# Kernel optimization log

Hardware: AMD Instinct MI355X
Metric: run time of the kernel (lower is better)

## Reference

```python
import jax, jax.numpy as jnp
import numpy as np

N, E, F, H, G = 50000, 640000, 128, 128, 64


def setup_inputs() -> dict:
    key = jax.random.key(0)
    ks = jax.random.split(key, 10)
    x = jax.random.normal(ks[0], (N, F), dtype=jnp.float32)
    edge_index = jax.random.randint(ks[1], (2, E), 0, N)
    batch = jnp.sort(jax.random.randint(ks[2], (N,), 0, G))

    def glorot(k, shp):
        return jax.random.normal(k, shp, dtype=jnp.float32) * np.float32(1.0 / np.sqrt(shp[0]))

    W1 = glorot(ks[3], (F, H)); b1 = jnp.zeros((H,), jnp.float32)
    W2 = glorot(ks[4], (H, H)); b2 = jnp.zeros((H,), jnp.float32)
    W3 = glorot(ks[5], (H, H)); b3 = jnp.zeros((H,), jnp.float32)
    W4 = glorot(ks[6], (H, 2)); b4 = jnp.zeros((2,), jnp.float32)
    return {"x": x, "W1": W1, "b1": b1, "W2": W2, "b2": b2,
            "W3": W3, "b3": b3, "W4": W4, "b4": b4,
            "edge_index": edge_index, "batch": batch, "num_graphs": G}


def reference(x, W1, b1, W2, b2, W3, b3, W4, b4, edge_index, batch, num_graphs):
    n = x.shape[0]
    loop = jnp.arange(n, dtype=edge_index.dtype)
    src = jnp.concatenate([edge_index[0], loop])  # with self-loops (PyG GCNConv default)
    dst = jnp.concatenate([edge_index[1], loop])
    # symmetric degree normalization: D^{-1/2} (A+I) D^{-1/2}
    deg = jax.ops.segment_sum(jnp.ones_like(src, dtype=x.dtype), dst, num_segments=n)
    dinv = jnp.where(deg > 0, jax.lax.rsqrt(deg), 0.0)
    norm = (dinv[src] * dinv[dst])[:, None]  # [E+N, 1]

    def gcn_conv(h, W, b):
        m = h @ W                                   # transform first (F->H), then propagate
        agg = jax.ops.segment_sum(m[src] * norm, dst, num_segments=n)
        return agg + b

    h = jax.nn.relu(gcn_conv(x, W1, b1))
    h = jax.nn.relu(gcn_conv(h, W2, b2))
    g = jax.ops.segment_max(h, batch, num_segments=num_graphs)  # global_max_pool
    z = jax.nn.relu(g @ W3 + b3)                    # dropout is identity in eval
    logits = z @ W4 + b4
    return jax.nn.log_softmax(logits, axis=1)
```

## Files before the change

kernel.cpp:

```cpp
#include <hip/hip_runtime.h>
#include <hip/hip_bf16.h>
#include <math.h>

#define HDIM 128
#define SCAN_B 256
#define NBLK 256

typedef short bfrag __attribute__((ext_vector_type(8)));
typedef float f32x4 __attribute__((ext_vector_type(4)));

__device__ inline unsigned short f2bf_rne(float x) {
    unsigned u = __float_as_uint(x);
    u = (u + 0x7fffu + ((u >> 16) & 1u)) >> 16;
    return (unsigned short)u;
}
__device__ inline float bf_lo(unsigned u) { return __uint_as_float(u << 16); }
__device__ inline float bf_hi(unsigned u) { return __uint_as_float(u & 0xffff0000u); }
__device__ inline unsigned bf_pack(float lo, float hi) {
    return ((unsigned)f2bf_rne(hi) << 16) | (unsigned)f2bf_rne(lo);
}


__device__ inline void hist_body(int b, const int* __restrict__ dst,
                                 int* __restrict__ hist, int E, int chunk, int nbuck) {
    __shared__ int hl[256];
    int t = threadIdx.x;
    hl[t] = 0;
    __syncthreads();
    int start = b * chunk, end = min(E, start + chunk);
    for (int e = start + t; e < end; e += 256) atomicAdd(&hl[dst[e] >> 8], 1);
    __syncthreads();
    if (t < nbuck) hist[t * NBLK + b] = hl[t];
}

__device__ inline void wfrag_body(int b, const float* __restrict__ W1,
                                  const float* __restrict__ W2,
                                  unsigned short* __restrict__ w1h,
                                  unsigned short* __restrict__ w1l,
                                  unsigned short* __restrict__ w2h,
                                  unsigned short* __restrict__ w2l) {
    const float* W = (b < 64) ? W1 : W2;
    unsigned short* whi = (b < 64) ? w1h : w2h;
    unsigned short* wlo = (b < 64) ? w1l : w2l;
    int idx = (b & 63) * 256 + threadIdx.x;
    int k = idx >> 7;
    int n = idx & 127;
    int kt = k >> 5, q = (k >> 3) & 3, j = k & 7;
    int lm = n >> 3, nt = n & 7;
    int lane = q * 16 + lm;
    int o = ((kt * 8 + nt) * 64 + lane) * 8 + j;
    float x = W[idx];
    unsigned short hb = f2bf_rne(x);
    float hf = __uint_as_float(((unsigned)hb) << 16);
    unsigned short lb = f2bf_rne(x - hf);
    whi[o] = hb;
    wlo[o] = lb;
}

__device__ inline void scatter_body(int b, const int* __restrict__ srcv,
                                    const int* __restrict__ dstv,
                                    const int* __restrict__ hscan,
                                    int2* __restrict__ sorted,
                                    int E, int chunk, int nbuck) {
    __shared__ int cur[256];
    int t = threadIdx.x;
    if (t < nbuck) cur[t] = hscan[t * NBLK + b];
    __syncthreads();
    int start = b * chunk, end = min(E, start + chunk);
    for (int e = start + t; e < end; e += 256) {
        int d = dstv[e];
        int pos = atomicAdd(&cur[d >> 8], 1);
        sorted[pos] = make_int2(srcv[e], d);
    }
}

#define GBM 64
__device__ inline void gemm_f32_body(int b, const float* __restrict__ A,
                                     const unsigned short* __restrict__ whi,
                                     const unsigned short* __restrict__ wlo,
                                     unsigned short* __restrict__ C, int Nrows) {
    int tid = threadIdx.x;
    int w = tid >> 6, L = tid & 63;
    int lm = L & 15, lq = L >> 4;
    int row0 = b * GBM + w * 16;

    f32x4 acc[8];
#pragma unroll
    for (int nt = 0; nt < 8; ++nt) acc[nt] = (f32x4)(0.f);

#pragma unroll
    for (int kt = 0; kt < 4; ++kt) {
        int gr = row0 + lm;
        float4 v0 = make_float4(0.f, 0.f, 0.f, 0.f);
        float4 v1 = v0;
        if (gr < Nrows) {
            const float* p = &A[(size_t)gr * HDIM + kt * 32 + lq * 8];
            v0 = *(const float4*)p;
            v1 = *(const float4*)(p + 4);
        }
        float xv[8] = {v0.x, v0.y, v0.z, v0.w, v1.x, v1.y, v1.z, v1.w};
        bfrag ah, al;
#pragma unroll
        for (int j = 0; j < 8; ++j) {
            float x = xv[j];
            unsigned short hb = f2bf_rne(x);
            float hf = __uint_as_float(((unsigned)hb) << 16);
            unsigned short lb = f2bf_rne(x - hf);
            ah[j] = (short)hb;
            al[j] = (short)lb;
        }
#pragma unroll
        for (int nt = 0; nt < 8; ++nt) {
            int o = ((kt * 8 + nt) * 64 + L) * 8;
            bfrag wh = *(const bfrag*)&whi[o];
            bfrag wl = *(const bfrag*)&wlo[o];
            acc[nt] = __builtin_amdgcn_mfma_f32_16x16x32_bf16(ah, wh, acc[nt], 0, 0, 0);
            acc[nt] = __builtin_amdgcn_mfma_f32_16x16x32_bf16(al, wh, acc[nt], 0, 0, 0);
            acc[nt] = __builtin_amdgcn_mfma_f32_16x16x32_bf16(ah, wl, acc[nt], 0, 0, 0);
        }
    }

#pragma unroll
    for (int i = 0; i < 4; ++i) {
        int gr = row0 + lq * 4 + i;
        if (gr < Nrows) {
            bfrag e;
#pragma unroll
            for (int nt = 0; nt < 8; ++nt) e[nt] = (short)f2bf_rne(acc[nt][i]);
            *(bfrag*)&C[(size_t)gr * HDIM + lm * 8] = e;
        }
    }
}

__global__ __launch_bounds__(256) void mega1_kernel(const int* __restrict__ dst,
                                                    int* __restrict__ hist, int E,
                                                    int chunk, int nbuck,
                                                    const float* __restrict__ W1,
                                                    const float* __restrict__ W2,
                                                    unsigned short* __restrict__ w1h,
                                                    unsigned short* __restrict__ w1l,
                                                    unsigned short* __restrict__ w2h,
                                                    unsigned short* __restrict__ w2l) {
    int b = blockIdx.x;
    if (b < NBLK) hist_body(b, dst, hist, E, chunk, nbuck);
    else wfrag_body(b - NBLK, W1, W2, w1h, w1l, w2h, w2l);
}

__global__ __launch_bounds__(256) void mega3_kernel(const int* __restrict__ srcv,
                                                    const int* __restrict__ dstv,
                                                    const int* __restrict__ hscan,
                                                    int2* __restrict__ sorted,
                                                    int E, int chunk, int nbuck,
                                                    const float* __restrict__ A,
                                                    const unsigned short* __restrict__ whi,
                                                    const unsigned short* __restrict__ wlo,
                                                    unsigned short* __restrict__ C, int Nrows) {
    int b = blockIdx.x;
    if (b < NBLK) scatter_body(b, srcv, dstv, hscan, sorted, E, chunk, nbuck);
    else gemm_f32_body(b - NBLK, A, whi, wlo, C, Nrows);
}

__global__ __launch_bounds__(SCAN_B) void scan1_kernel(const int* __restrict__ in,
                                                       int* __restrict__ out,
                                                       int* __restrict__ sums, int n) {
    __shared__ int s[SCAN_B];
    int t = threadIdx.x;
    int idx = blockIdx.x * SCAN_B + t;
    int v = (idx < n) ? in[idx] : 0;
    s[t] = v;
    __syncthreads();
    for (int off = 1; off < SCAN_B; off <<= 1) {
        int x = (t >= off) ? s[t - off] : 0;
        __syncthreads();
        s[t] += x;
        __syncthreads();
    }
    if (idx < n) out[idx] = s[t];
    if (t == SCAN_B - 1) sums[blockIdx.x] = s[t];
}

__global__ __launch_bounds__(SCAN_B) void scan2_kernel(int* __restrict__ sums, int nb) {
    __shared__ int s[SCAN_B];
    int t = threadIdx.x;
    int v = (t < nb) ? sums[t] : 0;
    s[t] = v;
    __syncthreads();
    for (int off = 1; off < SCAN_B; off <<= 1) {
        int x = (t >= off) ? s[t - off] : 0;
        __syncthreads();
        s[t] += x;
        __syncthreads();
    }
    if (t < nb) sums[t] = s[t] - v;
}

__global__ __launch_bounds__(SCAN_B) void scan3_kernel(const int* __restrict__ in,
                                                       int* __restrict__ out,
                                                       const int* __restrict__ sums, int n) {
    int idx = blockIdx.x * SCAN_B + threadIdx.x;
    if (idx < n) out[idx] = out[idx] - in[idx] + sums[blockIdx.x];
}

__global__ __launch_bounds__(256) void csr_kernel(const int2* __restrict__ sorted,
                                                  const int* __restrict__ hscan,
                                                  int* __restrict__ rowstart,
                                                  float* __restrict__ dinv,
                                                  int* __restrict__ csr,
                                                  int N, int E, int nbuck) {
    __shared__ int cnt[256];
    __shared__ int s[256];
    __shared__ int cur[256];
    int b = blockIdx.x;
    int t = threadIdx.x;
    int start = hscan[b * NBLK];
    int end = (b + 1 < nbuck) ? hscan[(b + 1) * NBLK] : E;
    cnt[t] = 0;
    __syncthreads();
    for (int e = start + t; e < end; e += 256)
        atomicAdd(&cnt[sorted[e].y & 255], 1);
    __syncthreads();
    int v = cnt[t];
    s[t] = v;
    __syncthreads();
    for (int off = 1; off < 256; off <<= 1) {
        int x = (t >= off) ? s[t - off] : 0;
        __syncthreads();
        s[t] += x;
        __syncthreads();
    }
    int excl = s[t] - v;
    int node = b * 256 + t;
    if (node < N) {
        rowstart[node] = start + excl;
        dinv[node] = rsqrtf((float)(v + 1));
    }
    if (b == nbuck - 1 && t == 0) rowstart[N] = E;
    cur[t] = start + excl;
    __syncthreads();
    for (int e = start + t; e < end; e += 256) {
        int2 ed = sorted[e];
        int pos = atomicAdd(&cur[ed.y & 255], 1);
        csr[pos] = ed.x;
    }
}

#define QACC(UV, WT)                                   \
    acc[0] = fmaf(WT, bf_lo((UV).x), acc[0]);          \
    acc[1] = fmaf(WT, bf_hi((UV).x), acc[1]);          \
    acc[2] = fmaf(WT, bf_lo((UV).y), acc[2]);          \
    acc[3] = fmaf(WT, bf_hi((UV).y), acc[3]);          \
    acc[4] = fmaf(WT, bf_lo((UV).z), acc[4]);          \
    acc[5] = fmaf(WT, bf_hi((UV).z), acc[5]);          \
    acc[6] = fmaf(WT, bf_lo((UV).w), acc[6]);          \
    acc[7] = fmaf(WT, bf_hi((UV).w), acc[7]);

__device__ inline void qgather(const uint4* __restrict__ m4,
                               const int* __restrict__ csr,
                               const float* __restrict__ dinv,
                               int p, int pend, int t, float* acc) {
    for (; p + 8 <= pend; p += 8) {
        int s0 = csr[p], s1 = csr[p + 1], s2 = csr[p + 2], s3 = csr[p + 3];
        int s4 = csr[p + 4], s5 = csr[p + 5], s6 = csr[p + 6], s7 = csr[p + 7];
        float w0 = dinv[s0], w1 = dinv[s1], w2 = dinv[s2], w3 = dinv[s3];
        float w4 = dinv[s4], w5 = dinv[s5], w6 = dinv[s6], w7 = dinv[s7];
        uint4 u0 = m4[(size_t)s0 * 16 + t];
        uint4 u1 = m4[(size_t)s1 * 16 + t];
        uint4 u2 = m4[(size_t)s2 * 16 + t];
        uint4 u3 = m4[(size_t)s3 * 16 + t];
        uint4 u4 = m4[(size_t)s4 * 16 + t];
        uint4 u5 = m4[(size_t)s5 * 16 + t];
        uint4 u6 = m4[(size_t)s6 * 16 + t];
        uint4 u7 = m4[(size_t)s7 * 16 + t];
        QACC(u0, w0); QACC(u1, w1); QACC(u2, w2); QACC(u3, w3);
        QACC(u4, w4); QACC(u5, w5); QACC(u6, w6); QACC(u7, w7);
    }
    if (p + 4 <= pend) {
        int s0 = csr[p], s1 = csr[p + 1], s2 = csr[p + 2], s3 = csr[p + 3];
        float w0 = dinv[s0], w1 = dinv[s1], w2 = dinv[s2], w3 = dinv[s3];
        uint4 u0 = m4[(size_t)s0 * 16 + t];
        uint4 u1 = m4[(size_t)s1 * 16 + t];
        uint4 u2 = m4[(size_t)s2 * 16 + t];
        uint4 u3 = m4[(size_t)s3 * 16 + t];
        QACC(u0, w0); QACC(u1, w1); QACC(u2, w2); QACC(u3, w3);
        p += 4;
    }
    if (p + 2 <= pend) {
        int s0 = csr[p], s1 = csr[p + 1];
        float w0 = dinv[s0], w1 = dinv[s1];
        uint4 u0 = m4[(size_t)s0 * 16 + t];
        uint4 u1 = m4[(size_t)s1 * 16 + t];
        QACC(u0, w0); QACC(u1, w1);
        p += 2;
    }
    if (p < pend) {
        int s0 = csr[p];
        float w0 = dinv[s0];
        uint4 u0 = m4[(size_t)s0 * 16 + t];
        QACC(u0, w0);
    }
}

__global__ __launch_bounds__(256) void agg_gemm_kernel(
        const uint4* __restrict__ m4,
        const int* __restrict__ rowstart,
        const int* __restrict__ csr,
        const float* __restrict__ dinv,
        const float* __restrict__ bias,
        const unsigned short* __restrict__ whi,
        const unsigned short* __restrict__ wlo,
        uint4* __restrict__ out_m, int n) {
    __shared__ unsigned short hbuf[16][HDIM + 8];
    __shared__ float cbuf[16][HDIM + 4];
    int t = threadIdx.x & 15;
    int nl = threadIdx.x >> 4;
    int node = blockIdx.x * 16 + nl;

    unsigned short hv[8] = {0, 0, 0, 0, 0, 0, 0, 0};
    if (node < n) {
        float dd = dinv[node];
        float acc[8];
        uint4 u = m4[(size_t)node * 16 + t];
        acc[0] = dd * bf_lo(u.x); acc[1] = dd * bf_hi(u.x);
        acc[2] = dd * bf_lo(u.y); acc[3] = dd * bf_hi(u.y);
        acc[4] = dd * bf_lo(u.z); acc[5] = dd * bf_hi(u.z);
        acc[6] = dd * bf_lo(u.w); acc[7] = dd * bf_hi(u.w);
        qgather(m4, csr, dinv, rowstart[node], rowstart[node + 1], t, acc);
        float4 b0 = *(const float4*)&bias[t * 8];
        float4 b1 = *(const float4*)&bias[t * 8 + 4];
        float bb[8] = {b0.x, b0.y, b0.z, b0.w, b1.x, b1.y, b1.z, b1.w};
#pragma unroll
        for (int j = 0; j < 8; ++j)
            hv[j] = f2bf_rne(fmaxf(fmaf(dd, acc[j], bb[j]), 0.f));
    }
    *(uint4*)&hbuf[nl][t * 8] = *(uint4*)hv;
    __syncthreads();

    int w = threadIdx.x >> 6, L = threadIdx.x & 63;
    int lm = L & 15, lq = L >> 4;
    f32x4 acc2[2];
    acc2[0] = (f32x4)(0.f);
    acc2[1] = (f32x4)(0.f);
#pragma unroll
    for (int kt = 0; kt < 4; ++kt) {
        bfrag a = *(const bfrag*)&hbuf[lm][kt * 32 + lq * 8];
#pragma unroll
        for (int q2 = 0; q2 < 2; ++q2) {
            int nt = w * 2 + q2;
            int o = ((kt * 8 + nt) * 64 + L) * 8;
            bfrag wh = *(const bfrag*)&whi[o];
            bfrag wl = *(const bfrag*)&wlo[o];
            acc2[q2] = __builtin_amdgcn_mfma_f32_16x16x32_bf16(a, wh, acc2[q2], 0, 0, 0);
            acc2[q2] = __builtin_amdgcn_mfma_f32_16x16x32_bf16(a, wl, acc2[q2], 0, 0, 0);
        }
    }
#pragma unroll
    for (int q2 = 0; q2 < 2; ++q2) {
        int nt = w * 2 + q2;
#pragma unroll
        for (int i = 0; i < 4; ++i) cbuf[lq * 4 + i][lm * 8 + nt] = acc2[q2][i];
    }
    __syncthreads();

    if (node < n) {
        float4 r0 = *(const float4*)&cbuf[nl][t * 8];
        float4 r1 = *(const float4*)&cbuf[nl][t * 8 + 4];
        unsigned short ev[8];
        ev[0] = f2bf_rne(r0.x); ev[1] = f2bf_rne(r0.y);
        ev[2] = f2bf_rne(r0.z); ev[3] = f2bf_rne(r0.w);
        ev[4] = f2bf_rne(r1.x); ev[5] = f2bf_rne(r1.y);
        ev[6] = f2bf_rne(r1.z); ev[7] = f2bf_rne(r1.w);
        out_m[(size_t)node * 16 + t] = *(uint4*)ev;
    }
}

__global__ __launch_bounds__(256) void agg_pool_kernel(const uint4* __restrict__ m4,
                                                       const int* __restrict__ rowstart,
                                                       const int* __restrict__ csr,
                                                       const float* __restrict__ dinv,
                                                       const float* __restrict__ bias,
                                                       const int* __restrict__ batch,
                                                       unsigned int* __restrict__ g, int n) {
    __shared__ float smx[16][HDIM];
    __shared__ int sgid[16];
    int t = threadIdx.x & 15;
    int nl = threadIdx.x >> 4;
    int node = blockIdx.x * 16 + nl;
    bool valid = node < n;
    if (valid) {
        float dd = dinv[node];
        float acc[8];
        uint4 u = m4[(size_t)node * 16 + t];
        acc[0] = dd * bf_lo(u.x); acc[1] = dd * bf_hi(u.x);
        acc[2] = dd * bf_lo(u.y); acc[3] = dd * bf_hi(u.y);
        acc[4] = dd * bf_lo(u.z); acc[5] = dd * bf_hi(u.z);
        acc[6] = dd * bf_lo(u.w); acc[7] = dd * bf_hi(u.w);
        qgather(m4, csr, dinv, rowstart[node], rowstart[node + 1], t, acc);
        float4 b0 = *(const float4*)&bias[t * 8];
        float4 b1 = *(const float4*)&bias[t * 8 + 4];
        float4 r0, r1;
        r0.x = fmaxf(fmaf(dd, acc[0], b0.x), 0.f);
        r0.y = fmaxf(fmaf(dd, acc[1], b0.y), 0.f);
        r0.z = fmaxf(fmaf(dd, acc[2], b0.z), 0.f);
        r0.w = fmaxf(fmaf(dd, acc[3], b0.w), 0.f);
        r1.x = fmaxf(fmaf(dd, acc[4], b1.x), 0.f);
        r1.y = fmaxf(fmaf(dd, acc[5], b1.y), 0.f);
        r1.z = fmaxf(fmaf(dd, acc[6], b1.z), 0.f);
        r1.w = fmaxf(fmaf(dd, acc[7], b1.w), 0.f);
        *(float4*)&smx[nl][t * 8] = r0;
        *(float4*)&smx[nl][t * 8 + 4] = r1;
    }
    if (t == 0) sgid[nl] = valid ? batch[node] : -1;
    __syncthreads();
    if (threadIdx.x < HDIM) {
        int c = threadIdx.x;
        int curg = -1;
        float run = 0.f;
#pragma unroll
        for (int r = 0; r < 16; ++r) {
            int gg = sgid[r];
            if (gg < 0) continue;
            if (gg != curg) {
                if (curg >= 0) atomicMax(&g[curg * HDIM + c], __float_as_uint(run));
                curg = gg;
                run = smx[r][c];
            } else {
                run = fmaxf(run, smx[r][c]);
            }
        }
        if (curg >= 0) atomicMax(&g[curg * HDIM + c], __float_as_uint(run));
    }
}

__global__ __launch_bounds__(128) void mlp_kernel(const unsigned int* __restrict__ gbits,
                                                  const float* __restrict__ W3,
                                                  const float* __restrict__ b3,
                                                  const float* __restrict__ W4,
                                                  const float* __restrict__ b4,
                                                  float* __restrict__ out) {
    __shared__ float gs[HDIM];
    __shared__ float r0[HDIM];
    __shared__ float r1[HDIM];
    int j = threadIdx.x;
    int b = blockIdx.x;
    gs[j] = __uint_as_float(gbits[b * HDIM + j]);
    __syncthreads();
    float acc = b3[j];
#pragma unroll 8
    for (int k = 0; k < HDIM; ++k) acc = fmaf(gs[k], W3[k * HDIM + j], acc);
    float z = fmaxf(acc, 0.f);
    r0[j] = z * W4[j * 2 + 0];
    r1[j] = z * W4[j * 2 + 1];
    __syncthreads();
    for (int off = 64; off > 0; off >>= 1) {
        if (j < off) {
            r0[j] += r0[j + off];
            r1[j] += r1[j + off];
        }
        __syncthreads();
    }
    if (j == 0) {
        float l0 = r0[0] + b4[0];
        float l1 = r1[0] + b4[1];
        float mx = fmaxf(l0, l1);
        float lse = mx + logf(expf(l0 - mx) + expf(l1 - mx));
        out[b * 2 + 0] = l0 - lse;
        out[b * 2 + 1] = l1 - lse;
    }
}

extern "C" void kernel_launch(void* const* d_in, const int* in_sizes, int n_in,
                              void* d_out, int out_size, void* d_ws, size_t ws_size,
                              hipStream_t stream) {
    const float* x  = (const float*)d_in[0];
    const float* W1 = (const float*)d_in[1];
    const float* b1 = (const float*)d_in[2];
    const float* W2 = (const float*)d_in[3];
    const float* b2 = (const float*)d_in[4];
    const float* W3 = (const float*)d_in[5];
    const float* b3 = (const float*)d_in[6];
    const float* W4 = (const float*)d_in[7];
    const float* b4 = (const float*)d_in[8];
    const int* ei    = (const int*)d_in[9];
    const int* batch = (const int*)d_in[10];

    const int N = in_sizes[0] / HDIM;
    const int E = in_sizes[9] / 2;
    const int G = out_size / 2;
    const int* src = ei;
    const int* dst = ei + E;

    const int nbuck = (N + 255) >> 8;
    const int nscan = nbuck * NBLK;
    const int chunk = (E + NBLK - 1) / NBLK;

    const int Nr = ((N + 63) / 64) * 64;
    char* wsb = (char*)d_ws;
    size_t o = 0;
    unsigned int* g = (unsigned int*)(wsb + o); o += (size_t)G * HDIM * 4;
    size_t zero_bytes = o;
    int* hist = (int*)(wsb + o);           o += (size_t)nscan * 4;
    int* hscan = (int*)(wsb + o);          o += (size_t)nscan * 4;
    int* sums = (int*)(wsb + o);           o += 256 * 4;
    int* rowstart = (int*)(wsb + o);       o += (size_t)(Nr + 64) * 4;
    float* dinv = (float*)(wsb + o);       o += (size_t)Nr * 4;
    int2* sorted = (int2*)(wsb + o);       o += (size_t)E * 8;
    int* csr = (int*)(wsb + o);            o += (size_t)E * 4;
    unsigned short* wf1h = (unsigned short*)(wsb + o); o += (size_t)HDIM * HDIM * 2;
    unsigned short* wf1l = (unsigned short*)(wsb + o); o += (size_t)HDIM * HDIM * 2;
    unsigned short* wf2h = (unsigned short*)(wsb + o); o += (size_t)HDIM * HDIM * 2;
    unsigned short* wf2l = (unsigned short*)(wsb + o); o += (size_t)HDIM * HDIM * 2;
    unsigned short* m = (unsigned short*)(wsb + o);    o += (size_t)Nr * HDIM * 2;
    unsigned short* m2 = (unsigned short*)(wsb + o);   o += (size_t)Nr * HDIM * 2;
    (void)ws_size; (void)n_in;

    (void)hipMemsetAsync(d_ws, 0, zero_bytes, stream);

    int sblocks = (nscan + SCAN_B - 1) / SCAN_B;
    int gemm_blocks = (N + GBM - 1) / GBM;
    int agg_blocks = (N + 15) / 16;

    mega1_kernel<<<NBLK + 128, 256, 0, stream>>>(dst, hist, E, chunk, nbuck,
                                                 W1, W2, wf1h, wf1l, wf2h, wf2l);
    scan1_kernel<<<sblocks, SCAN_B, 0, stream>>>(hist, hscan, sums, nscan);
    scan2_kernel<<<1, SCAN_B, 0, stream>>>(sums, sblocks);
    scan3_kernel<<<sblocks, SCAN_B, 0, stream>>>(hist, hscan, sums, nscan);
    mega3_kernel<<<NBLK + gemm_blocks, 256, 0, stream>>>(src, dst, hscan, sorted,
                                                         E, chunk, nbuck,
                                                         x, wf1h, wf1l, m, N);
    csr_kernel<<<nbuck, 256, 0, stream>>>(sorted, hscan, rowstart, dinv, csr, N, E, nbuck);
    agg_gemm_kernel<<<agg_blocks, 256, 0, stream>>>((const uint4*)m, rowstart, csr,
                                                    dinv, b1, wf2h, wf2l,
                                                    (uint4*)m2, N);
    agg_pool_kernel<<<agg_blocks, 256, 0, stream>>>((const uint4*)m2, rowstart, csr,
                                                    dinv, b2, batch, g, N);
    mlp_kernel<<<G, 128, 0, stream>>>(g, W3, b3, W4, b4, (float*)d_out);
}
```

Baseline: 201.4 us.

## Build CSR with direct global atomics and prescale messages by source dinv

```diff
diff --git a/kernel.cpp b/kernel.cpp
--- a/kernel.cpp
+++ b/kernel.cpp
@@ -16,21 +16,13 @@
 }
 __device__ inline float bf_lo(unsigned u) { return __uint_as_float(u << 16); }
 __device__ inline float bf_hi(unsigned u) { return __uint_as_float(u & 0xffff0000u); }
-__device__ inline unsigned bf_pack(float lo, float hi) {
-    return ((unsigned)f2bf_rne(hi) << 16) | (unsigned)f2bf_rne(lo);
-}
 
 
 __device__ inline void hist_body(int b, const int* __restrict__ dst,
-                                 int* __restrict__ hist, int E, int chunk, int nbuck) {
-    __shared__ int hl[256];
-    int t = threadIdx.x;
-    hl[t] = 0;
-    __syncthreads();
+                                 int* __restrict__ hist, int E, int chunk) {
     int start = b * chunk, end = min(E, start + chunk);
-    for (int e = start + t; e < end; e += 256) atomicAdd(&hl[dst[e] >> 8], 1);
-    __syncthreads();
-    if (t < nbuck) hist[t * NBLK + b] = hl[t];
+    for (int e = start + threadIdx.x; e < end; e += 256)
+        atomicAdd(&hist[dst[e]], 1);
 }
 
 __device__ inline void wfrag_body(int b, const float* __restrict__ W1,
@@ -59,18 +51,13 @@
 
 __device__ inline void scatter_body(int b, const int* __restrict__ srcv,
                                     const int* __restrict__ dstv,
-                                    const int* __restrict__ hscan,
-                                    int2* __restrict__ sorted,
-                                    int E, int chunk, int nbuck) {
-    __shared__ int cur[256];
-    int t = threadIdx.x;
-    if (t < nbuck) cur[t] = hscan[t * NBLK + b];
-    __syncthreads();
+                                    int* __restrict__ cursor,
+                                    int* __restrict__ csr,
+                                    int E, int chunk) {
     int start = b * chunk, end = min(E, start + chunk);
-    for (int e = start + t; e < end; e += 256) {
-        int d = dstv[e];
-        int pos = atomicAdd(&cur[d >> 8], 1);
-        sorted[pos] = make_int2(srcv[e], d);
+    for (int e = start + threadIdx.x; e < end; e += 256) {
+        int pos = atomicAdd(&cursor[dstv[e]], 1);
+        csr[pos] = srcv[e];
     }
 }
 
@@ -78,6 +65,7 @@
 __device__ inline void gemm_f32_body(int b, const float* __restrict__ A,
                                      const unsigned short* __restrict__ whi,
                                      const unsigned short* __restrict__ wlo,
+                                     const float* __restrict__ dinv,
                                      unsigned short* __restrict__ C, int Nrows) {
     int tid = threadIdx.x;
     int w = tid >> 6, L = tid & 63;
@@ -124,9 +112,10 @@
     for (int i = 0; i < 4; ++i) {
         int gr = row0 + lq * 4 + i;
         if (gr < Nrows) {
+            float dd = dinv[gr];
             bfrag e;
 #pragma unroll
-            for (int nt = 0; nt < 8; ++nt) e[nt] = (short)f2bf_rne(acc[nt][i]);
+            for (int nt = 0; nt < 8; ++nt) e[nt] = (short)f2bf_rne(dd * acc[nt][i]);
             *(bfrag*)&C[(size_t)gr * HDIM + lm * 8] = e;
         }
     }
@@ -134,7 +123,7 @@
 
 __global__ __launch_bounds__(256) void mega1_kernel(const int* __restrict__ dst,
                                                     int* __restrict__ hist, int E,
-                                                    int chunk, int nbuck,
+                                                    int chunk,
                                                     const float* __restrict__ W1,
                                                     const float* __restrict__ W2,
                                                     unsigned short* __restrict__ w1h,
@@ -142,22 +131,23 @@
                                                     unsigned short* __restrict__ w2h,
                                                     unsigned short* __restrict__ w2l) {
     int b = blockIdx.x;
-    if (b < NBLK) hist_body(b, dst, hist, E, chunk, nbuck);
+    if (b < NBLK) hist_body(b, dst, hist, E, chunk);
     else wfrag_body(b - NBLK, W1, W2, w1h, w1l, w2h, w2l);
 }
 
 __global__ __launch_bounds__(256) void mega3_kernel(const int* __restrict__ srcv,
                                                     const int* __restrict__ dstv,
-                                                    const int* __restrict__ hscan,
-                                                    int2* __restrict__ sorted,
-                                                    int E, int chunk, int nbuck,
+                                                    int* __restrict__ cursor,
+                                                    int* __restrict__ csr,
+                                                    int E, int chunk,
                                                     const float* __restrict__ A,
                                                     const unsigned short* __restrict__ whi,
                                                     const unsigned short* __restrict__ wlo,
+                                                    const float* __restrict__ dinv,
                                                     unsigned short* __restrict__ C, int Nrows) {
     int b = blockIdx.x;
-    if (b < NBLK) scatter_body(b, srcv, dstv, hscan, sorted, E, chunk, nbuck);
-    else gemm_f32_body(b - NBLK, A, whi, wlo, C, Nrows);
+    if (b < NBLK) scatter_body(b, srcv, dstv, cursor, csr, E, chunk);
+    else gemm_f32_body(b - NBLK, A, whi, wlo, dinv, C, Nrows);
 }
 
 __global__ __launch_bounds__(SCAN_B) void scan1_kernel(const int* __restrict__ in,
@@ -179,90 +169,46 @@
     if (t == SCAN_B - 1) sums[blockIdx.x] = s[t];
 }
 
-__global__ __launch_bounds__(SCAN_B) void scan2_kernel(int* __restrict__ sums, int nb) {
+__global__ __launch_bounds__(SCAN_B) void scan3_kernel(const int* __restrict__ in,
+                                                       const int* __restrict__ incl,
+                                                       const int* __restrict__ sums,
+                                                       int* __restrict__ rowstart,
+                                                       int* __restrict__ cursor,
+                                                       float* __restrict__ dinv,
+                                                       int n, int E) {
     __shared__ int s[SCAN_B];
     int t = threadIdx.x;
-    int v = (t < nb) ? sums[t] : 0;
-    s[t] = v;
-    __syncthreads();
-    for (int off = 1; off < SCAN_B; off <<= 1) {
-        int x = (t >= off) ? s[t - off] : 0;
+    int b = blockIdx.x;
+    s[t] = (t < b) ? sums[t] : 0;
+    __syncthreads();
+    for (int off = SCAN_B / 2; off > 0; off >>= 1) {
+        if (t < off) s[t] += s[t + off];
         __syncthreads();
-        s[t] += x;
-        __syncthreads();
-    }
-    if (t < nb) sums[t] = s[t] - v;
-}
-
-__global__ __launch_bounds__(SCAN_B) void scan3_kernel(const int* __restrict__ in,
-                                                       int* __restrict__ out,
-                                                       const int* __restrict__ sums, int n) {
-    int idx = blockIdx.x * SCAN_B + threadIdx.x;
-    if (idx < n) out[idx] = out[idx] - in[idx] + sums[blockIdx.x];
-}
-
-__global__ __launch_bounds__(256) void csr_kernel(const int2* __restrict__ sorted,
-                                                  const int* __restrict__ hscan,
-                                                  int* __restrict__ rowstart,
-                                                  float* __restrict__ dinv,
-                                                  int* __restrict__ csr,
-                                                  int N, int E, int nbuck) {
-    __shared__ int cnt[256];
-    __shared__ int s[256];
-    __shared__ int cur[256];
-    int b = blockIdx.x;
-    int t = threadIdx.x;
-    int start = hscan[b * NBLK];
-    int end = (b + 1 < nbuck) ? hscan[(b + 1) * NBLK] : E;
-    cnt[t] = 0;
-    __syncthreads();
-    for (int e = start + t; e < end; e += 256)
-        atomicAdd(&cnt[sorted[e].y & 255], 1);
-    __syncthreads();
-    int v = cnt[t];
-    s[t] = v;
-    __syncthreads();
-    for (int off = 1; off < 256; off <<= 1) {
-        int x = (t >= off) ? s[t - off] : 0;
-        __syncthreads();
-        s[t] += x;
-        __syncthreads();
-    }
-    int excl = s[t] - v;
-    int node = b * 256 + t;
-    if (node < N) {
-        rowstart[node] = start + excl;
-        dinv[node] = rsqrtf((float)(v + 1));
-    }
-    if (b == nbuck - 1 && t == 0) rowstart[N] = E;
-    cur[t] = start + excl;
-    __syncthreads();
-    for (int e = start + t; e < end; e += 256) {
-        int2 ed = sorted[e];
-        int pos = atomicAdd(&cur[ed.y & 255], 1);
-        csr[pos] = ed.x;
-    }
-}
-
-#define QACC(UV, WT)                                   \
-    acc[0] = fmaf(WT, bf_lo((UV).x), acc[0]);          \
-    acc[1] = fmaf(WT, bf_hi((UV).x), acc[1]);          \
-    acc[2] = fmaf(WT, bf_lo((UV).y), acc[2]);          \
-    acc[3] = fmaf(WT, bf_hi((UV).y), acc[3]);          \
-    acc[4] = fmaf(WT, bf_lo((UV).z), acc[4]);          \
-    acc[5] = fmaf(WT, bf_hi((UV).z), acc[5]);          \
-    acc[6] = fmaf(WT, bf_lo((UV).w), acc[6]);          \
-    acc[7] = fmaf(WT, bf_hi((UV).w), acc[7]);
+    }
+    int base = s[0];
+    int idx = b * SCAN_B + t;
+    if (idx < n) {
+        int d = in[idx];
+        int excl = incl[idx] - d + base;
+        rowstart[idx] = excl;
+        cursor[idx] = excl;
+        dinv[idx] = rsqrtf((float)(d + 1));
+        if (idx == n - 1) rowstart[idx + 1] = E;
+    }
+}
+
+#define QACC(UV)                                       \
+    acc[0] += bf_lo((UV).x); acc[1] += bf_hi((UV).x);  \
+    acc[2] += bf_lo((UV).y); acc[3] += bf_hi((UV).y);  \
+    acc[4] += bf_lo((UV).z); acc[5] += bf_hi((UV).z);  \
+    acc[6] += bf_lo((UV).w); acc[7] += bf_hi((UV).w);
 
 __device__ inline void qgather(const uint4* __restrict__ m4,
                                const int* __restrict__ csr,
-                               const float* __restrict__ dinv,
                                int p, int pend, int t, float* acc) {
     for (; p + 8 <= pend; p += 8) {
         int s0 = csr[p], s1 = csr[p + 1], s2 = csr[p + 2], s3 = csr[p + 3];
         int s4 = csr[p + 4], s5 = csr[p + 5], s6 = csr[p + 6], s7 = csr[p + 7];
-        float w0 = dinv[s0], w1 = dinv[s1], w2 = dinv[s2], w3 = dinv[s3];
-        float w4 = dinv[s4], w5 = dinv[s5], w6 = dinv[s6], w7 = dinv[s7];
         uint4 u0 = m4[(size_t)s0 * 16 + t];
         uint4 u1 = m4[(size_t)s1 * 16 + t];
         uint4 u2 = m4[(size_t)s2 * 16 + t];
@@ -271,32 +217,29 @@
         uint4 u5 = m4[(size_t)s5 * 16 + t];
         uint4 u6 = m4[(size_t)s6 * 16 + t];
         uint4 u7 = m4[(size_t)s7 * 16 + t];
-        QACC(u0, w0); QACC(u1, w1); QACC(u2, w2); QACC(u3, w3);
-        QACC(u4, w4); QACC(u5, w5); QACC(u6, w6); QACC(u7, w7);
+        QACC(u0); QACC(u1); QACC(u2); QACC(u3);
+        QACC(u4); QACC(u5); QACC(u6); QACC(u7);
     }
     if (p + 4 <= pend) {
         int s0 = csr[p], s1 = csr[p + 1], s2 = csr[p + 2], s3 = csr[p + 3];
-        float w0 = dinv[s0], w1 = dinv[s1], w2 = dinv[s2], w3 = dinv[s3];
         uint4 u0 = m4[(size_t)s0 * 16 + t];
         uint4 u1 = m4[(size_t)s1 * 16 + t];
         uint4 u2 = m4[(size_t)s2 * 16 + t];
         uint4 u3 = m4[(size_t)s3 * 16 + t];
-        QACC(u0, w0); QACC(u1, w1); QACC(u2, w2); QACC(u3, w3);
+        QACC(u0); QACC(u1); QACC(u2); QACC(u3);
         p += 4;
     }
     if (p + 2 <= pend) {
         int s0 = csr[p], s1 = csr[p + 1];
-        float w0 = dinv[s0], w1 = dinv[s1];
         uint4 u0 = m4[(size_t)s0 * 16 + t];
         uint4 u1 = m4[(size_t)s1 * 16 + t];
-        QACC(u0, w0); QACC(u1, w1);
+        QACC(u0); QACC(u1);
         p += 2;
     }
     if (p < pend) {
         int s0 = csr[p];
-        float w0 = dinv[s0];
         uint4 u0 = m4[(size_t)s0 * 16 + t];
-        QACC(u0, w0);
+        QACC(u0);
     }
 }
 
@@ -315,16 +258,17 @@
     int nl = threadIdx.x >> 4;
     int node = blockIdx.x * 16 + nl;
 
+    float dd = 0.f;
     unsigned short hv[8] = {0, 0, 0, 0, 0, 0, 0, 0};
     if (node < n) {
-        float dd = dinv[node];
+        dd = dinv[node];
         float acc[8];
         uint4 u = m4[(size_t)node * 16 + t];
-        acc[0] = dd * bf_lo(u.x); acc[1] = dd * bf_hi(u.x);
-        acc[2] = dd * bf_lo(u.y); acc[3] = dd * bf_hi(u.y);
-        acc[4] = dd * bf_lo(u.z); acc[5] = dd * bf_hi(u.z);
-        acc[6] = dd * bf_lo(u.w); acc[7] = dd * bf_hi(u.w);
-        qgather(m4, csr, dinv, rowstart[node], rowstart[node + 1], t, acc);
+        acc[0] = bf_lo(u.x); acc[1] = bf_hi(u.x);
+        acc[2] = bf_lo(u.y); acc[3] = bf_hi(u.y);
+        acc[4] = bf_lo(u.z); acc[5] = bf_hi(u.z);
+        acc[6] = bf_lo(u.w); acc[7] = bf_hi(u.w);
+        qgather(m4, csr, rowstart[node], rowstart[node + 1], t, acc);
         float4 b0 = *(const float4*)&bias[t * 8];
         float4 b1 = *(const float4*)&bias[t * 8 + 4];
         float bb[8] = {b0.x, b0.y, b0.z, b0.w, b1.x, b1.y, b1.z, b1.w};
@@ -365,10 +309,10 @@
         float4 r0 = *(const float4*)&cbuf[nl][t * 8];
         float4 r1 = *(const float4*)&cbuf[nl][t * 8 + 4];
         unsigned short ev[8];
-        ev[0] = f2bf_rne(r0.x); ev[1] = f2bf_rne(r0.y);
-        ev[2] = f2bf_rne(r0.z); ev[3] = f2bf_rne(r0.w);
-        ev[4] = f2bf_rne(r1.x); ev[5] = f2bf_rne(r1.y);
-        ev[6] = f2bf_rne(r1.z); ev[7] = f2bf_rne(r1.w);
+        ev[0] = f2bf_rne(dd * r0.x); ev[1] = f2bf_rne(dd * r0.y);
+        ev[2] = f2bf_rne(dd * r0.z); ev[3] = f2bf_rne(dd * r0.w);
+        ev[4] = f2bf_rne(dd * r1.x); ev[5] = f2bf_rne(dd * r1.y);
+        ev[6] = f2bf_rne(dd * r1.z); ev[7] = f2bf_rne(dd * r1.w);
         out_m[(size_t)node * 16 + t] = *(uint4*)ev;
     }
 }
@@ -390,11 +334,11 @@
         float dd = dinv[node];
         float acc[8];
         uint4 u = m4[(size_t)node * 16 + t];
-        acc[0] = dd * bf_lo(u.x); acc[1] = dd * bf_hi(u.x);
-        acc[2] = dd * bf_lo(u.y); acc[3] = dd * bf_hi(u.y);
-        acc[4] = dd * bf_lo(u.z); acc[5] = dd * bf_hi(u.z);
-        acc[6] = dd * bf_lo(u.w); acc[7] = dd * bf_hi(u.w);
-        qgather(m4, csr, dinv, rowstart[node], rowstart[node + 1], t, acc);
+        acc[0] = bf_lo(u.x); acc[1] = bf_hi(u.x);
+        acc[2] = bf_lo(u.y); acc[3] = bf_hi(u.y);
+        acc[4] = bf_lo(u.z); acc[5] = bf_hi(u.z);
+        acc[6] = bf_lo(u.w); acc[7] = bf_hi(u.w);
+        qgather(m4, csr, rowstart[node], rowstart[node + 1], t, acc);
         float4 b0 = *(const float4*)&bias[t * 8];
         float4 b1 = *(const float4*)&bias[t * 8 + 4];
         float4 r0, r1;
@@ -489,21 +433,19 @@
     const int* src = ei;
     const int* dst = ei + E;
 
-    const int nbuck = (N + 255) >> 8;
-    const int nscan = nbuck * NBLK;
     const int chunk = (E + NBLK - 1) / NBLK;
 
     const int Nr = ((N + 63) / 64) * 64;
     char* wsb = (char*)d_ws;
     size_t o = 0;
     unsigned int* g = (unsigned int*)(wsb + o); o += (size_t)G * HDIM * 4;
+    int* hist = (int*)(wsb + o);           o += (size_t)Nr * 4;
     size_t zero_bytes = o;
-    int* hist = (int*)(wsb + o);           o += (size_t)nscan * 4;
-    int* hscan = (int*)(wsb + o);          o += (size_t)nscan * 4;
+    int* hscan = (int*)(wsb + o);          o += (size_t)Nr * 4;
     int* sums = (int*)(wsb + o);           o += 256 * 4;
     int* rowstart = (int*)(wsb + o);       o += (size_t)(Nr + 64) * 4;
+    int* cursor = (int*)(wsb + o);         o += (size_t)Nr * 4;
     float* dinv = (float*)(wsb + o);       o += (size_t)Nr * 4;
-    int2* sorted = (int2*)(wsb + o);       o += (size_t)E * 8;
     int* csr = (int*)(wsb + o);            o += (size_t)E * 4;
     unsigned short* wf1h = (unsigned short*)(wsb + o); o += (size_t)HDIM * HDIM * 2;
     unsigned short* wf1l = (unsigned short*)(wsb + o); o += (size_t)HDIM * HDIM * 2;
@@ -515,19 +457,18 @@
 
     (void)hipMemsetAsync(d_ws, 0, zero_bytes, stream);
 
-    int sblocks = (nscan + SCAN_B - 1) / SCAN_B;
+    int sblocks = (N + SCAN_B - 1) / SCAN_B;
     int gemm_blocks = (N + GBM - 1) / GBM;
     int agg_blocks = (N + 15) / 16;
 
-    mega1_kernel<<<NBLK + 128, 256, 0, stream>>>(dst, hist, E, chunk, nbuck,
+    mega1_kernel<<<NBLK + 128, 256, 0, stream>>>(dst, hist, E, chunk,
                                                  W1, W2, wf1h, wf1l, wf2h, wf2l);
-    scan1_kernel<<<sblocks, SCAN_B, 0, stream>>>(hist, hscan, sums, nscan);
-    scan2_kernel<<<1, SCAN_B, 0, stream>>>(sums, sblocks);
-    scan3_kernel<<<sblocks, SCAN_B, 0, stream>>>(hist, hscan, sums, nscan);
-    mega3_kernel<<<NBLK + gemm_blocks, 256, 0, stream>>>(src, dst, hscan, sorted,
-                                                         E, chunk, nbuck,
-                                                         x, wf1h, wf1l, m, N);
-    csr_kernel<<<nbuck, 256, 0, stream>>>(sorted, hscan, rowstart, dinv, csr, N, E, nbuck);
+    scan1_kernel<<<sblocks, SCAN_B, 0, stream>>>(hist, hscan, sums, N);
+    scan3_kernel<<<sblocks, SCAN_B, 0, stream>>>(hist, hscan, sums,
+                                                 rowstart, cursor, dinv, N, E);
+    mega3_kernel<<<NBLK + gemm_blocks, 256, 0, stream>>>(src, dst, cursor, csr,
+                                                         E, chunk,
+                                                         x, wf1h, wf1l, dinv, m, N);
     agg_gemm_kernel<<<agg_blocks, 256, 0, stream>>>((const uint4*)m, rowstart, csr,
                                                     dinv, b1, wf2h, wf2l,
                                                     (uint4*)m2, N);
```

Result: slower. 228.9 us (+13.7%).

## Degree-sort nodes within aggregation blocks, prescale layer-2 messages, merge scan passes

Applied to the files above, without the earlier changes.

```diff
diff --git a/kernel.cpp b/kernel.cpp
--- a/kernel.cpp
+++ b/kernel.cpp
@@ -16,9 +16,6 @@
 }
 __device__ inline float bf_lo(unsigned u) { return __uint_as_float(u << 16); }
 __device__ inline float bf_hi(unsigned u) { return __uint_as_float(u & 0xffff0000u); }
-__device__ inline unsigned bf_pack(float lo, float hi) {
-    return ((unsigned)f2bf_rne(hi) << 16) | (unsigned)f2bf_rne(lo);
-}
 
 
 __device__ inline void hist_body(int b, const int* __restrict__ dst,
@@ -179,26 +176,22 @@
     if (t == SCAN_B - 1) sums[blockIdx.x] = s[t];
 }
 
-__global__ __launch_bounds__(SCAN_B) void scan2_kernel(int* __restrict__ sums, int nb) {
+__global__ __launch_bounds__(SCAN_B) void scan3_kernel(const int* __restrict__ in,
+                                                       int* __restrict__ inout,
+                                                       const int* __restrict__ sums,
+                                                       int n) {
     __shared__ int s[SCAN_B];
     int t = threadIdx.x;
-    int v = (t < nb) ? sums[t] : 0;
-    s[t] = v;
-    __syncthreads();
-    for (int off = 1; off < SCAN_B; off <<= 1) {
-        int x = (t >= off) ? s[t - off] : 0;
+    int b = blockIdx.x;
+    s[t] = (t < b) ? sums[t] : 0;
+    __syncthreads();
+    for (int off = SCAN_B / 2; off > 0; off >>= 1) {
+        if (t < off) s[t] += s[t + off];
         __syncthreads();
-        s[t] += x;
-        __syncthreads();
-    }
-    if (t < nb) sums[t] = s[t] - v;
-}
-
-__global__ __launch_bounds__(SCAN_B) void scan3_kernel(const int* __restrict__ in,
-                                                       int* __restrict__ out,
-                                                       const int* __restrict__ sums, int n) {
-    int idx = blockIdx.x * SCAN_B + threadIdx.x;
-    if (idx < n) out[idx] = out[idx] - in[idx] + sums[blockIdx.x];
+    }
+    int base = s[0];
+    int idx = b * SCAN_B + t;
+    if (idx < n) inout[idx] = inout[idx] - in[idx] + base;
 }
 
 __global__ __launch_bounds__(256) void csr_kernel(const int2* __restrict__ sorted,
@@ -244,16 +237,26 @@
     }
 }
 
-#define QACC(UV, WT)                                   \
-    acc[0] = fmaf(WT, bf_lo((UV).x), acc[0]);          \
-    acc[1] = fmaf(WT, bf_hi((UV).x), acc[1]);          \
-    acc[2] = fmaf(WT, bf_lo((UV).y), acc[2]);          \
-    acc[3] = fmaf(WT, bf_hi((UV).y), acc[3]);          \
-    acc[4] = fmaf(WT, bf_lo((UV).z), acc[4]);          \
-    acc[5] = fmaf(WT, bf_hi((UV).z), acc[5]);          \
-    acc[6] = fmaf(WT, bf_lo((UV).w), acc[6]);          \
-    acc[7] = fmaf(WT, bf_hi((UV).w), acc[7]);
-
+template <bool W>
+__device__ inline void qacc(float* acc, uint4 uv, float wt) {
+    if (W) {
+        acc[0] = fmaf(wt, bf_lo(uv.x), acc[0]);
+        acc[1] = fmaf(wt, bf_hi(uv.x), acc[1]);
+        acc[2] = fmaf(wt, bf_lo(uv.y), acc[2]);
+        acc[3] = fmaf(wt, bf_hi(uv.y), acc[3]);
+        acc[4] = fmaf(wt, bf_lo(uv.z), acc[4]);
+        acc[5] = fmaf(wt, bf_hi(uv.z), acc[5]);
+        acc[6] = fmaf(wt, bf_lo(uv.w), acc[6]);
+        acc[7] = fmaf(wt, bf_hi(uv.w), acc[7]);
+    } else {
+        acc[0] += bf_lo(uv.x); acc[1] += bf_hi(uv.x);
+        acc[2] += bf_lo(uv.y); acc[3] += bf_hi(uv.y);
+        acc[4] += bf_lo(uv.z); acc[5] += bf_hi(uv.z);
+        acc[6] += bf_lo(uv.w); acc[7] += bf_hi(uv.w);
+    }
+}
+
+template <bool W>
 __device__ inline void qgather(const uint4* __restrict__ m4,
                                const int* __restrict__ csr,
                                const float* __restrict__ dinv,
@@ -261,8 +264,12 @@
     for (; p + 8 <= pend; p += 8) {
         int s0 = csr[p], s1 = csr[p + 1], s2 = csr[p + 2], s3 = csr[p + 3];
         int s4 = csr[p + 4], s5 = csr[p + 5], s6 = csr[p + 6], s7 = csr[p + 7];
-        float w0 = dinv[s0], w1 = dinv[s1], w2 = dinv[s2], w3 = dinv[s3];
-        float w4 = dinv[s4], w5 = dinv[s5], w6 = dinv[s6], w7 = dinv[s7];
+        float w0 = 0.f, w1 = 0.f, w2 = 0.f, w3 = 0.f;
+        float w4 = 0.f, w5 = 0.f, w6 = 0.f, w7 = 0.f;
+        if (W) {
+            w0 = dinv[s0]; w1 = dinv[s1]; w2 = dinv[s2]; w3 = dinv[s3];
+            w4 = dinv[s4]; w5 = dinv[s5]; w6 = dinv[s6]; w7 = dinv[s7];
+        }
         uint4 u0 = m4[(size_t)s0 * 16 + t];
         uint4 u1 = m4[(size_t)s1 * 16 + t];
         uint4 u2 = m4[(size_t)s2 * 16 + t];
@@ -271,33 +278,59 @@
         uint4 u5 = m4[(size_t)s5 * 16 + t];
         uint4 u6 = m4[(size_t)s6 * 16 + t];
         uint4 u7 = m4[(size_t)s7 * 16 + t];
-        QACC(u0, w0); QACC(u1, w1); QACC(u2, w2); QACC(u3, w3);
-        QACC(u4, w4); QACC(u5, w5); QACC(u6, w6); QACC(u7, w7);
+        qacc<W>(acc, u0, w0); qacc<W>(acc, u1, w1);
+        qacc<W>(acc, u2, w2); qacc<W>(acc, u3, w3);
+        qacc<W>(acc, u4, w4); qacc<W>(acc, u5, w5);
+        qacc<W>(acc, u6, w6); qacc<W>(acc, u7, w7);
     }
     if (p + 4 <= pend) {
         int s0 = csr[p], s1 = csr[p + 1], s2 = csr[p + 2], s3 = csr[p + 3];
-        float w0 = dinv[s0], w1 = dinv[s1], w2 = dinv[s2], w3 = dinv[s3];
+        float w0 = 0.f, w1 = 0.f, w2 = 0.f, w3 = 0.f;
+        if (W) { w0 = dinv[s0]; w1 = dinv[s1]; w2 = dinv[s2]; w3 = dinv[s3]; }
         uint4 u0 = m4[(size_t)s0 * 16 + t];
         uint4 u1 = m4[(size_t)s1 * 16 + t];
         uint4 u2 = m4[(size_t)s2 * 16 + t];
         uint4 u3 = m4[(size_t)s3 * 16 + t];
-        QACC(u0, w0); QACC(u1, w1); QACC(u2, w2); QACC(u3, w3);
+        qacc<W>(acc, u0, w0); qacc<W>(acc, u1, w1);
+        qacc<W>(acc, u2, w2); qacc<W>(acc, u3, w3);
         p += 4;
     }
     if (p + 2 <= pend) {
         int s0 = csr[p], s1 = csr[p + 1];
-        float w0 = dinv[s0], w1 = dinv[s1];
+        float w0 = 0.f, w1 = 0.f;
+        if (W) { w0 = dinv[s0]; w1 = dinv[s1]; }
         uint4 u0 = m4[(size_t)s0 * 16 + t];
         uint4 u1 = m4[(size_t)s1 * 16 + t];
-        QACC(u0, w0); QACC(u1, w1);
+        qacc<W>(acc, u0, w0); qacc<W>(acc, u1, w1);
         p += 2;
     }
     if (p < pend) {
         int s0 = csr[p];
-        float w0 = dinv[s0];
+        float w0 = W ? dinv[s0] : 0.f;
         uint4 u0 = m4[(size_t)s0 * 16 + t];
-        QACC(u0, w0);
-    }
+        qacc<W>(acc, u0, w0);
+    }
+}
+
+__device__ inline int degree_perm(const int* __restrict__ rowstart,
+                                  int* lens, int* perm, int n) {
+    if (threadIdx.x < 16) {
+        int nn = blockIdx.x * 16 + threadIdx.x;
+        lens[threadIdx.x] = (nn < n) ? (rowstart[nn + 1] - rowstart[nn]) : -1;
+    }
+    __syncthreads();
+    if (threadIdx.x < 16) {
+        int L = lens[threadIdx.x];
+        int r = 0;
+#pragma unroll
+        for (int j = 0; j < 16; ++j) {
+            int Lj = lens[j];
+            r += (Lj > L || (Lj == L && j < (int)threadIdx.x)) ? 1 : 0;
+        }
+        perm[r] = threadIdx.x;
+    }
+    __syncthreads();
+    return perm[threadIdx.x >> 4];
 }
 
 __global__ __launch_bounds__(256) void agg_gemm_kernel(
@@ -311,9 +344,12 @@
         uint4* __restrict__ out_m, int n) {
     __shared__ unsigned short hbuf[16][HDIM + 8];
     __shared__ float cbuf[16][HDIM + 4];
+    __shared__ int lens[16];
+    __shared__ int perm[16];
     int t = threadIdx.x & 15;
-    int nl = threadIdx.x >> 4;
-    int node = blockIdx.x * 16 + nl;
+
+    int pnl = degree_perm(rowstart, lens, perm, n);
+    int node = blockIdx.x * 16 + pnl;
 
     unsigned short hv[8] = {0, 0, 0, 0, 0, 0, 0, 0};
     if (node < n) {
@@ -324,7 +360,7 @@
         acc[2] = dd * bf_lo(u.y); acc[3] = dd * bf_hi(u.y);
         acc[4] = dd * bf_lo(u.z); acc[5] = dd * bf_hi(u.z);
         acc[6] = dd * bf_lo(u.w); acc[7] = dd * bf_hi(u.w);
-        qgather(m4, csr, dinv, rowstart[node], rowstart[node + 1], t, acc);
+        qgather<true>(m4, csr, dinv, rowstart[node], rowstart[node + 1], t, acc);
         float4 b0 = *(const float4*)&bias[t * 8];
         float4 b1 = *(const float4*)&bias[t * 8 + 4];
         float bb[8] = {b0.x, b0.y, b0.z, b0.w, b1.x, b1.y, b1.z, b1.w};
@@ -332,7 +368,7 @@
         for (int j = 0; j < 8; ++j)
             hv[j] = f2bf_rne(fmaxf(fmaf(dd, acc[j], bb[j]), 0.f));
     }
-    *(uint4*)&hbuf[nl][t * 8] = *(uint4*)hv;
+    *(uint4*)&hbuf[pnl][t * 8] = *(uint4*)hv;
     __syncthreads();
 
     int w = threadIdx.x >> 6, L = threadIdx.x & 63;
@@ -361,15 +397,18 @@
     }
     __syncthreads();
 
-    if (node < n) {
+    int nl = threadIdx.x >> 4;
+    int node_e = blockIdx.x * 16 + nl;
+    if (node_e < n) {
+        float dde = dinv[node_e];
         float4 r0 = *(const float4*)&cbuf[nl][t * 8];
         float4 r1 = *(const float4*)&cbuf[nl][t * 8 + 4];
         unsigned short ev[8];
-        ev[0] = f2bf_rne(r0.x); ev[1] = f2bf_rne(r0.y);
-        ev[2] = f2bf_rne(r0.z); ev[3] = f2bf_rne(r0.w);
-        ev[4] = f2bf_rne(r1.x); ev[5] = f2bf_rne(r1.y);
-        ev[6] = f2bf_rne(r1.z); ev[7] = f2bf_rne(r1.w);
-        out_m[(size_t)node * 16 + t] = *(uint4*)ev;
+        ev[0] = f2bf_rne(dde * r0.x); ev[1] = f2bf_rne(dde * r0.y);
+        ev[2] = f2bf_rne(dde * r0.z); ev[3] = f2bf_rne(dde * r0.w);
+        ev[4] = f2bf_rne(dde * r1.x); ev[5] = f2bf_rne(dde * r1.y);
+        ev[6] = f2bf_rne(dde * r1.z); ev[7] = f2bf_rne(dde * r1.w);
+        out_m[(size_t)node_e * 16 + t] = *(uint4*)ev;
     }
 }
 
@@ -382,19 +421,22 @@
                                                        unsigned int* __restrict__ g, int n) {
     __shared__ float smx[16][HDIM];
     __shared__ int sgid[16];
+    __shared__ int lens[16];
+    __shared__ int perm[16];
     int t = threadIdx.x & 15;
-    int nl = threadIdx.x >> 4;
-    int node = blockIdx.x * 16 + nl;
+
+    int pnl = degree_perm(rowstart, lens, perm, n);
+    int node = blockIdx.x * 16 + pnl;
     bool valid = node < n;
     if (valid) {
         float dd = dinv[node];
         float acc[8];
         uint4 u = m4[(size_t)node * 16 + t];
-        acc[0] = dd * bf_lo(u.x); acc[1] = dd * bf_hi(u.x);
-        acc[2] = dd * bf_lo(u.y); acc[3] = dd * bf_hi(u.y);
-        acc[4] = dd * bf_lo(u.z); acc[5] = dd * bf_hi(u.z);
-        acc[6] = dd * bf_lo(u.w); acc[7] = dd * bf_hi(u.w);
-        qgather(m4, csr, dinv, rowstart[node], rowstart[node + 1], t, acc);
+        acc[0] = bf_lo(u.x); acc[1] = bf_hi(u.x);
+        acc[2] = bf_lo(u.y); acc[3] = bf_hi(u.y);
+        acc[4] = bf_lo(u.z); acc[5] = bf_hi(u.z);
+        acc[6] = bf_lo(u.w); acc[7] = bf_hi(u.w);
+        qgather<false>(m4, csr, dinv, rowstart[node], rowstart[node + 1], t, acc);
         float4 b0 = *(const float4*)&bias[t * 8];
         float4 b1 = *(const float4*)&bias[t * 8 + 4];
         float4 r0, r1;
@@ -406,10 +448,10 @@
         r1.y = fmaxf(fmaf(dd, acc[5], b1.y), 0.f);
         r1.z = fmaxf(fmaf(dd, acc[6], b1.z), 0.f);
         r1.w = fmaxf(fmaf(dd, acc[7], b1.w), 0.f);
-        *(float4*)&smx[nl][t * 8] = r0;
-        *(float4*)&smx[nl][t * 8 + 4] = r1;
-    }
-    if (t == 0) sgid[nl] = valid ? batch[node] : -1;
+        *(float4*)&smx[pnl][t * 8] = r0;
+        *(float4*)&smx[pnl][t * 8 + 4] = r1;
+    }
+    if (t == 0) sgid[pnl] = valid ? batch[node] : -1;
     __syncthreads();
     if (threadIdx.x < HDIM) {
         int c = threadIdx.x;
@@ -522,7 +564,6 @@
     mega1_kernel<<<NBLK + 128, 256, 0, stream>>>(dst, hist, E, chunk, nbuck,
                                                  W1, W2, wf1h, wf1l, wf2h, wf2l);
     scan1_kernel<<<sblocks, SCAN_B, 0, stream>>>(hist, hscan, sums, nscan);
-    scan2_kernel<<<1, SCAN_B, 0, stream>>>(sums, sblocks);
     scan3_kernel<<<sblocks, SCAN_B, 0, stream>>>(hist, hscan, sums, nscan);
     mega3_kernel<<<NBLK + gemm_blocks, 256, 0, stream>>>(src, dst, hscan, sorted,
                                                          E, chunk, nbuck,
```

After: 201.7 us. Within noise of the previous version (+0.2%).
